# Optimization experiments

Hardware: AMD Instinct MI355X
Metric: run time of the kernel (lower is better)

Reference implementation:

```python
import jax, jax.numpy as jnp
import numpy as np

B2, NC, DIM, H, W = 512, 16, 256, 16, 16


def setup_inputs() -> dict:
    key = jax.random.key(0)
    kf, kr, kc = jax.random.split(key, 3)
    features = jax.random.normal(kf, (B2, DIM, H, W), dtype=jnp.float32)
    # ranking rows are random permutations of class ids 0..NC-1
    perm_keys = jax.random.split(kr, B2)
    ranking = jax.vmap(lambda k: jax.random.permutation(k, NC))(perm_keys).astype(jnp.int32)
    # positive-threshold choice in [1, NC-1] so both arange steps are finite
    choice = jax.random.randint(kc, (B2,), 1, NC, dtype=jnp.int32)
    return {"features": features, "ranking": ranking, "choice": choice, "num_class": NC}


def reference(features, ranking, choice, num_class):
    b2 = features.shape[0]
    x = features.reshape(b2, -1)  # [b2, D]
    sq = jnp.sum(x * x, axis=1)
    dist2 = sq[:, None] + sq[None, :] - 2.0 * (x @ x.T)
    dist = jnp.sqrt(jnp.clip(dist2, 1e-12, None))  # [b2, b2]

    labels = ranking[:, 0]  # pseudo-label of each sample
    # pos[i, c] = rank position j of class c within ranking[i] (inverse permutation)
    pos = jnp.argsort(ranking, axis=1)  # [b2, nc]
    # rank_of_label[i, k] = rank of sample k's label within sample i's ranking
    rank_of_label = pos[:, labels]  # [b2, b2]

    # dic_s[j] = 1 - j/c            for j <  c   (torch.arange(1, 0, -1/c))
    #          = -(j - c + 1)/(nc-c) for j >= c   (torch.arange(-1/(nc-c), -1-1/(nc-c), -1/(nc-c)))
    c = choice[:, None].astype(dist.dtype)  # [b2, 1]
    j = rank_of_label.astype(dist.dtype)
    nc = jnp.asarray(num_class, dist.dtype)
    mask = jnp.where(rank_of_label < choice[:, None],
                     1.0 - j / c,
                     -(j - c + 1.0) / (nc - c))  # [b2, b2]
    # (initial eq-mask is fully overwritten because each ranking row is a full permutation)

    return jnp.mean((dist * mask) ** 2)
```

## Files before the change

kernel.cpp:

```cpp
#include <hip/hip_runtime.h>
#include <hip/hip_bf16.h>

typedef float f32x4 __attribute__((ext_vector_type(4)));
typedef __bf16 bf16x8 __attribute__((ext_vector_type(8)));

constexpr int B2     = 512;
constexpr int KDIM   = 65536;
constexpr int BM     = 256;
constexpr int BK     = 32;
constexpr int NK     = KDIM / BK;
constexpr int KSPLIT = 85;
constexpr int NBLK   = 3 * KSPLIT;

__device__ __forceinline__ void gload16(const void* g, void* l) {
    __builtin_amdgcn_global_load_lds(
        (__attribute__((address_space(1))) void*)(g),
        (__attribute__((address_space(3))) void*)(l), 16, 0, 0);
}

__device__ __forceinline__ void stage_panel(const float* __restrict__ src, int k0,
                                            float* ldsPanel, int tid) {
#pragma unroll
    for (int i = 0; i < 4; ++i) {
        int r    = i * 64 + (tid >> 3);
        int slot = (tid & 7) ^ (r & 7);
        const float* g = src + (size_t)r * KDIM + k0 + slot * 4;
        char* l = (char*)ldsPanel + i * 8192 + (tid & ~63) * 16;
        gload16(g, l);
    }
}

__device__ __forceinline__ bf16x8 read_frag(const char* base, int rowByte, int s0b, int s1b) {
    f32x4 lo = *reinterpret_cast<const f32x4*>(base + rowByte + s0b);
    f32x4 hi = *reinterpret_cast<const f32x4*>(base + rowByte + s1b);
    bf16x8 r;
    r[0] = (__bf16)lo[0]; r[1] = (__bf16)lo[1]; r[2] = (__bf16)lo[2]; r[3] = (__bf16)lo[3];
    r[4] = (__bf16)hi[0]; r[5] = (__bf16)hi[1]; r[6] = (__bf16)hi[2]; r[7] = (__bf16)hi[3];
    return r;
}

__global__ __launch_bounds__(512, 2) void gemm_partial(const float* __restrict__ X,
                                                       __bf16* __restrict__ partials) {
    __shared__ __align__(16) float ldsT[2][2][BM * BK];

    int d = blockIdx.x;
    int xcd = d & 7, slotb = d >> 3;
    int L = (xcd < 7 ? xcd * 32 : 224) + slotb;
    int split = L / 3;
    int tile  = L - split * 3;

    int ti = (tile == 2) ? 1 : 0;
    int tj = (tile == 0) ? 0 : 1;
    bool diag = (ti == tj);
    const float* Abase = X + (size_t)ti * 256 * KDIM;
    const float* Bbase = X + (size_t)tj * 256 * KDIM;

    int tid  = threadIdx.x;
    int lane = tid & 63;
    int wave = tid >> 6;
    int wr = wave >> 2, wc = wave & 3;

    int s0 = split * NK / KSPLIT;
    int s1 = (split + 1) * NK / KSPLIT;

    f32x4 acc[8][4] = {};

    int q  = lane >> 4;
    int rx = lane & 7;
    int s0b = ((2 * q)     ^ rx) * 16;
    int s1b = ((2 * q + 1) ^ rx) * 16;

    stage_panel(Abase, s0 * BK, &ldsT[0][0][0], tid);
    if (!diag) stage_panel(Bbase, s0 * BK, &ldsT[0][1][0], tid);
    __syncthreads();

    int cur = 0;
    for (int s = s0; s < s1; ++s) {
        if (s + 1 < s1) {
            stage_panel(Abase, (s + 1) * BK, &ldsT[cur ^ 1][0][0], tid);
            if (!diag) stage_panel(Bbase, (s + 1) * BK, &ldsT[cur ^ 1][1][0], tid);
        }

        const char* bA = (const char*)&ldsT[cur][0][0];
        const char* bB = diag ? bA : (const char*)&ldsT[cur][1][0];

        bf16x8 bfr[4];
#pragma unroll
        for (int ni = 0; ni < 4; ++ni) {
            int rowB = wc * 64 + ni * 16 + (lane & 15);
            bfr[ni] = read_frag(bB, rowB * 128, s0b, s1b);
        }
#pragma unroll
        for (int mi = 0; mi < 8; ++mi) {
            int rowA = wr * 128 + mi * 16 + (lane & 15);
            bf16x8 a = read_frag(bA, rowA * 128, s0b, s1b);
#pragma unroll
            for (int ni = 0; ni < 4; ++ni)
                acc[mi][ni] = __builtin_amdgcn_mfma_f32_16x16x32_bf16(
                    a, bfr[ni], acc[mi][ni], 0, 0, 0);
        }

        __syncthreads();
        cur ^= 1;
    }

    __bf16* out = partials + (size_t)(tile * KSPLIT + split) * (BM * BM);
    int col = lane & 15, rquad = (lane >> 4) * 4;
#pragma unroll
    for (int mi = 0; mi < 8; ++mi)
#pragma unroll
        for (int ni = 0; ni < 4; ++ni) {
            int j = wc * 64 + ni * 16 + col;
#pragma unroll
            for (int v = 0; v < 4; ++v) {
                int i = wr * 128 + mi * 16 + rquad + v;
                out[i * BM + j] = (__bf16)acc[mi][ni][v];
            }
        }
}

__global__ __launch_bounds__(256) void reduce_partials(const __bf16* __restrict__ partials,
                                                       float* __restrict__ C) {
    int idx  = blockIdx.x * 256 + threadIdx.x;
    int tile = idx / 16384;
    int e4   = idx & 16383;
    const __bf16* p = partials + (size_t)tile * KSPLIT * 65536 + e4 * 4;
    float sx = 0.f, sy = 0.f, sz = 0.f, sw = 0.f;
    for (int s = 0; s < KSPLIT; ++s) {
        ushort4 v = *reinterpret_cast<const ushort4*>(p + (size_t)s * 65536);
        union { unsigned u; float f; } a, b, c2, d2;
        a.u  = (unsigned)v.x << 16;  b.u  = (unsigned)v.y << 16;
        c2.u = (unsigned)v.z << 16;  d2.u = (unsigned)v.w << 16;
        sx += a.f; sy += b.f; sz += c2.f; sw += d2.f;
    }
    int e = e4 * 4;
    int i = e >> 8, j = e & 255;
    int gi = (tile == 2) ? 256 + i : i;
    int gj = (tile == 0) ? j : 256 + j;
    float4 sum = make_float4(sx, sy, sz, sw);
    *reinterpret_cast<float4*>(C + gi * 512 + gj) = sum;
    if (tile == 1) {
        C[(gj + 0) * 512 + gi] = sum.x;
        C[(gj + 1) * 512 + gi] = sum.y;
        C[(gj + 2) * 512 + gi] = sum.z;
        C[(gj + 3) * 512 + gi] = sum.w;
    }
}

__global__ __launch_bounds__(256) void loss_kernel(const float* __restrict__ C,
                                                   const int* __restrict__ ranking,
                                                   const int* __restrict__ choice,
                                                   const int* __restrict__ ncp,
                                                   float* __restrict__ out) {
    __shared__ int pos[16];
    __shared__ float wsum[4];
    int i   = blockIdx.x;
    int tid = threadIdx.x;
    if (tid < 16) pos[ranking[i * 16 + tid]] = tid;
    __syncthreads();

    float nc  = (float)(*ncp);
    int   ci  = choice[i];
    float c   = (float)ci;
    float sqi = C[i * 513];
    float sum = 0.f;

    for (int j = tid; j < B2; j += 256) {
        int   lbl = ranking[j * 16];
        int   r   = pos[lbl];
        float sqj = C[j * 513];
        float d2  = sqi + sqj - 2.f * C[i * 512 + j];
        d2 = fmaxf(d2, 1e-12f);
        float jf = (float)r;
        float m  = (r < ci) ? (1.f - jf / c) : (-(jf - c + 1.f) / (nc - c));
        sum += d2 * m * m;
    }

    for (int off = 32; off > 0; off >>= 1) sum += __shfl_down(sum, off);
    int lane = tid & 63, wave = tid >> 6;
    if (lane == 0) wsum[wave] = sum;
    __syncthreads();
    if (tid == 0) {
        float t = wsum[0] + wsum[1] + wsum[2] + wsum[3];
        atomicAdd(out, t * (1.f / ((float)B2 * (float)B2)));
    }
}

extern "C" void kernel_launch(void* const* d_in, const int* in_sizes, int n_in,
                              void* d_out, int out_size, void* d_ws, size_t ws_size,
                              hipStream_t stream) {
    const float* X       = (const float*)d_in[0];
    const int*   ranking = (const int*)d_in[1];
    const int*   choice  = (const int*)d_in[2];
    const int*   ncp     = (const int*)d_in[3];
    float*       ws      = (float*)d_ws;

    float*  C        = ws;
    __bf16* partials = (__bf16*)(ws + 262144);

    hipMemsetAsync(d_out, 0, sizeof(float), stream);

    gemm_partial<<<dim3(NBLK), dim3(512), 0, stream>>>(X, partials);
    reduce_partials<<<dim3(3 * 16384 / 256), dim3(256), 0, stream>>>(partials, C);
    loss_kernel<<<dim3(B2), dim3(256), 0, stream>>>(C, ranking, choice, ncp, (float*)d_out);
}
```

Measured before the change: 68.00 us.

## Retile Gram GEMM into 128x128 upper-triangle tiles with register-staged bf16 LDS

The 512x512 Gram product now uses ten 128x128 upper-triangular tiles, each split 76 ways along K, replacing three 256x256 tiles with 85 splits. Each block has 256 threads and is bounded to three blocks per CU. Panels are loaded from global memory into registers, converted to bf16 once, and written to a swizzled bf16 LDS buffer, replacing the fp32 direct-to-LDS loads that converted on every fragment read. This halves LDS footprint and adds a register prefetch two steps ahead. The trade-off is more re-reads of X across tiles, plus more partial buffers for the reduce kernel, which now handles the new tile mapping.

```diff
diff --git a/kernel.cpp b/kernel.cpp
--- a/kernel.cpp
+++ b/kernel.cpp
@@ -6,140 +6,144 @@
 
 constexpr int B2     = 512;
 constexpr int KDIM   = 65536;
-constexpr int BM     = 256;
+constexpr int TM     = 128;
 constexpr int BK     = 32;
 constexpr int NK     = KDIM / BK;
-constexpr int KSPLIT = 85;
-constexpr int NBLK   = 3 * KSPLIT;
-
-__device__ __forceinline__ void gload16(const void* g, void* l) {
-    __builtin_amdgcn_global_load_lds(
-        (__attribute__((address_space(1))) void*)(g),
-        (__attribute__((address_space(3))) void*)(l), 16, 0, 0);
-}
-
-__device__ __forceinline__ void stage_panel(const float* __restrict__ src, int k0,
-                                            float* ldsPanel, int tid) {
-#pragma unroll
-    for (int i = 0; i < 4; ++i) {
-        int r    = i * 64 + (tid >> 3);
-        int slot = (tid & 7) ^ (r & 7);
-        const float* g = src + (size_t)r * KDIM + k0 + slot * 4;
-        char* l = (char*)ldsPanel + i * 8192 + (tid & ~63) * 16;
-        gload16(g, l);
-    }
-}
-
-__device__ __forceinline__ bf16x8 read_frag(const char* base, int rowByte, int s0b, int s1b) {
-    f32x4 lo = *reinterpret_cast<const f32x4*>(base + rowByte + s0b);
-    f32x4 hi = *reinterpret_cast<const f32x4*>(base + rowByte + s1b);
-    bf16x8 r;
-    r[0] = (__bf16)lo[0]; r[1] = (__bf16)lo[1]; r[2] = (__bf16)lo[2]; r[3] = (__bf16)lo[3];
-    r[4] = (__bf16)hi[0]; r[5] = (__bf16)hi[1]; r[6] = (__bf16)hi[2]; r[7] = (__bf16)hi[3];
-    return r;
-}
-
-__global__ __launch_bounds__(512, 2) void gemm_partial(const float* __restrict__ X,
+constexpr int NTILE  = 10;
+constexpr int KSPLIT = 76;
+constexpr int NBLK   = NTILE * KSPLIT;
+
+__device__ __forceinline__ void issue_panel(float4* p, const float* __restrict__ src,
+                                            int k0, int tid) {
+    const float* g = src + (size_t)(tid >> 1) * KDIM + k0 + (tid & 1) * 16;
+#pragma unroll
+    for (int it = 0; it < 4; ++it)
+        p[it] = *reinterpret_cast<const float4*>(g + it * 4);
+}
+
+__device__ __forceinline__ void write_panel(__bf16* panel, const float4* p, int tid) {
+    int r = tid >> 1, h = tid & 1;
+    bf16x8 v0, v1;
+    v0[0] = (__bf16)p[0].x; v0[1] = (__bf16)p[0].y; v0[2] = (__bf16)p[0].z; v0[3] = (__bf16)p[0].w;
+    v0[4] = (__bf16)p[1].x; v0[5] = (__bf16)p[1].y; v0[6] = (__bf16)p[1].z; v0[7] = (__bf16)p[1].w;
+    v1[0] = (__bf16)p[2].x; v1[1] = (__bf16)p[2].y; v1[2] = (__bf16)p[2].z; v1[3] = (__bf16)p[2].w;
+    v1[4] = (__bf16)p[3].x; v1[5] = (__bf16)p[3].y; v1[6] = (__bf16)p[3].z; v1[7] = (__bf16)p[3].w;
+    char* base = reinterpret_cast<char*>(panel) + r * 64;
+    *reinterpret_cast<bf16x8*>(base + (((2 * h)     ^ (r & 3)) * 16)) = v0;
+    *reinterpret_cast<bf16x8*>(base + (((2 * h + 1) ^ (r & 3)) * 16)) = v1;
+}
+
+__device__ __forceinline__ void lds_barrier() {
+    asm volatile("s_waitcnt lgkmcnt(0)" ::: "memory");
+    __builtin_amdgcn_s_barrier();
+}
+
+__global__ __launch_bounds__(256, 3) void gemm_partial(const float* __restrict__ X,
                                                        __bf16* __restrict__ partials) {
-    __shared__ __align__(16) float ldsT[2][2][BM * BK];
+    __shared__ __align__(16) __bf16 lds[2][2][TM * BK];
 
     int d = blockIdx.x;
-    int xcd = d & 7, slotb = d >> 3;
-    int L = (xcd < 7 ? xcd * 32 : 224) + slotb;
-    int split = L / 3;
-    int tile  = L - split * 3;
-
-    int ti = (tile == 2) ? 1 : 0;
-    int tj = (tile == 0) ? 0 : 1;
-    bool diag = (ti == tj);
-    const float* Abase = X + (size_t)ti * 256 * KDIM;
-    const float* Bbase = X + (size_t)tj * 256 * KDIM;
+    int L = (d & 7) * 95 + (d >> 3);
+    int split = L / NTILE;
+    int t     = L - split * NTILE;
+    int i = (t >= 9) ? 3 : (t >= 7) ? 2 : (t >= 4) ? 1 : 0;
+    int j = t - ((i == 0) ? 0 : (i == 1) ? 3 : (i == 2) ? 5 : 6);
+    bool diag = (i == j);
+    const float* Abase = X + (size_t)i * TM * KDIM;
+    const float* Bbase = X + (size_t)j * TM * KDIM;
 
     int tid  = threadIdx.x;
     int lane = tid & 63;
     int wave = tid >> 6;
-    int wr = wave >> 2, wc = wave & 3;
+    int wr = wave >> 1, wc = wave & 1;
 
     int s0 = split * NK / KSPLIT;
     int s1 = (split + 1) * NK / KSPLIT;
 
-    f32x4 acc[8][4] = {};
-
-    int q  = lane >> 4;
-    int rx = lane & 7;
-    int s0b = ((2 * q)     ^ rx) * 16;
-    int s1b = ((2 * q + 1) ^ rx) * 16;
-
-    stage_panel(Abase, s0 * BK, &ldsT[0][0][0], tid);
-    if (!diag) stage_panel(Bbase, s0 * BK, &ldsT[0][1][0], tid);
-    __syncthreads();
-
-    int cur = 0;
+    f32x4 acc[4][4] = {};
+    float4 pa[4], pb[4];
+
+    int pslot  = ((lane >> 4) ^ (lane & 3)) * 16;
+    int rbyteA = (wr * 64 + (lane & 15)) * 64 + pslot;
+    int rbyteB = (wc * 64 + (lane & 15)) * 64 + pslot;
+
+    issue_panel(pa, Abase, s0 * BK, tid);
+    if (!diag) issue_panel(pb, Bbase, s0 * BK, tid);
+    write_panel(&lds[0][0][0], pa, tid);
+    if (!diag) write_panel(&lds[0][1][0], pb, tid);
+    if (s0 + 1 < s1) {
+        issue_panel(pa, Abase, (s0 + 1) * BK, tid);
+        if (!diag) issue_panel(pb, Bbase, (s0 + 1) * BK, tid);
+    }
+    lds_barrier();
+
     for (int s = s0; s < s1; ++s) {
-        if (s + 1 < s1) {
-            stage_panel(Abase, (s + 1) * BK, &ldsT[cur ^ 1][0][0], tid);
-            if (!diag) stage_panel(Bbase, (s + 1) * BK, &ldsT[cur ^ 1][1][0], tid);
-        }
-
-        const char* bA = (const char*)&ldsT[cur][0][0];
-        const char* bB = diag ? bA : (const char*)&ldsT[cur][1][0];
+        int cur = (s - s0) & 1;
+        const char* bA = (const char*)&lds[cur][0][0];
+        const char* bB = diag ? bA : (const char*)&lds[cur][1][0];
 
         bf16x8 bfr[4];
 #pragma unroll
-        for (int ni = 0; ni < 4; ++ni) {
-            int rowB = wc * 64 + ni * 16 + (lane & 15);
-            bfr[ni] = read_frag(bB, rowB * 128, s0b, s1b);
-        }
-#pragma unroll
-        for (int mi = 0; mi < 8; ++mi) {
-            int rowA = wr * 128 + mi * 16 + (lane & 15);
-            bf16x8 a = read_frag(bA, rowA * 128, s0b, s1b);
+        for (int ni = 0; ni < 4; ++ni)
+            bfr[ni] = *reinterpret_cast<const bf16x8*>(bB + rbyteB + ni * 1024);
+#pragma unroll
+        for (int mi = 0; mi < 4; ++mi) {
+            bf16x8 a = *reinterpret_cast<const bf16x8*>(bA + rbyteA + mi * 1024);
 #pragma unroll
             for (int ni = 0; ni < 4; ++ni)
                 acc[mi][ni] = __builtin_amdgcn_mfma_f32_16x16x32_bf16(
                     a, bfr[ni], acc[mi][ni], 0, 0, 0);
         }
 
-        __syncthreads();
-        cur ^= 1;
-    }
-
-    __bf16* out = partials + (size_t)(tile * KSPLIT + split) * (BM * BM);
-    int col = lane & 15, rquad = (lane >> 4) * 4;
-#pragma unroll
-    for (int mi = 0; mi < 8; ++mi)
-#pragma unroll
-        for (int ni = 0; ni < 4; ++ni) {
-            int j = wc * 64 + ni * 16 + col;
-#pragma unroll
-            for (int v = 0; v < 4; ++v) {
-                int i = wr * 128 + mi * 16 + rquad + v;
-                out[i * BM + j] = (__bf16)acc[mi][ni][v];
+        if (s + 1 < s1) {
+            write_panel(&lds[cur ^ 1][0][0], pa, tid);
+            if (!diag) write_panel(&lds[cur ^ 1][1][0], pb, tid);
+            if (s + 2 < s1) {
+                issue_panel(pa, Abase, (s + 2) * BK, tid);
+                if (!diag) issue_panel(pb, Bbase, (s + 2) * BK, tid);
             }
         }
+        lds_barrier();
+    }
+
+    __bf16* out = partials + (size_t)(t * KSPLIT + split) * (TM * TM);
+    int col = lane & 15, rquad = (lane >> 4) * 4;
+#pragma unroll
+    for (int mi = 0; mi < 4; ++mi)
+#pragma unroll
+        for (int ni = 0; ni < 4; ++ni) {
+            int cj = wc * 64 + ni * 16 + col;
+#pragma unroll
+            for (int v = 0; v < 4; ++v) {
+                int ri = wr * 64 + mi * 16 + rquad + v;
+                out[ri * TM + cj] = (__bf16)acc[mi][ni][v];
+            }
+        }
 }
 
 __global__ __launch_bounds__(256) void reduce_partials(const __bf16* __restrict__ partials,
                                                        float* __restrict__ C) {
-    int idx  = blockIdx.x * 256 + threadIdx.x;
-    int tile = idx / 16384;
-    int e4   = idx & 16383;
-    const __bf16* p = partials + (size_t)tile * KSPLIT * 65536 + e4 * 4;
+    int idx = blockIdx.x * 256 + threadIdx.x;
+    int t   = idx / 4096;
+    int e4  = idx & 4095;
+    int r   = e4 >> 5;
+    int c4  = e4 & 31;
+    const __bf16* src = partials + (size_t)t * KSPLIT * (TM * TM) + r * TM + c4 * 4;
     float sx = 0.f, sy = 0.f, sz = 0.f, sw = 0.f;
     for (int s = 0; s < KSPLIT; ++s) {
-        ushort4 v = *reinterpret_cast<const ushort4*>(p + (size_t)s * 65536);
+        ushort4 v = *reinterpret_cast<const ushort4*>(src + (size_t)s * (TM * TM));
         union { unsigned u; float f; } a, b, c2, d2;
         a.u  = (unsigned)v.x << 16;  b.u  = (unsigned)v.y << 16;
         c2.u = (unsigned)v.z << 16;  d2.u = (unsigned)v.w << 16;
         sx += a.f; sy += b.f; sz += c2.f; sw += d2.f;
     }
-    int e = e4 * 4;
-    int i = e >> 8, j = e & 255;
-    int gi = (tile == 2) ? 256 + i : i;
-    int gj = (tile == 0) ? j : 256 + j;
+    int i = (t >= 9) ? 3 : (t >= 7) ? 2 : (t >= 4) ? 1 : 0;
+    int j = t - ((i == 0) ? 0 : (i == 1) ? 3 : (i == 2) ? 5 : 6);
+    int gi = i * TM + r;
+    int gj = j * TM + c4 * 4;
     float4 sum = make_float4(sx, sy, sz, sw);
     *reinterpret_cast<float4*>(C + gi * 512 + gj) = sum;
-    if (tile == 1) {
+    if (i != j) {
         C[(gj + 0) * 512 + gi] = sum.x;
         C[(gj + 1) * 512 + gi] = sum.y;
         C[(gj + 2) * 512 + gi] = sum.z;
@@ -181,8 +185,8 @@
     if (lane == 0) wsum[wave] = sum;
     __syncthreads();
     if (tid == 0) {
-        float t = wsum[0] + wsum[1] + wsum[2] + wsum[3];
-        atomicAdd(out, t * (1.f / ((float)B2 * (float)B2)));
+        float tsum = wsum[0] + wsum[1] + wsum[2] + wsum[3];
+        atomicAdd(out, tsum * (1.f / ((float)B2 * (float)B2)));
     }
 }
 
@@ -200,7 +204,7 @@
 
     hipMemsetAsync(d_out, 0, sizeof(float), stream);
 
-    gemm_partial<<<dim3(NBLK), dim3(512), 0, stream>>>(X, partials);
-    reduce_partials<<<dim3(3 * 16384 / 256), dim3(256), 0, stream>>>(partials, C);
+    gemm_partial<<<dim3(NBLK), dim3(256), 0, stream>>>(X, partials);
+    reduce_partials<<<dim3(NTILE * 4096 / 256), dim3(256), 0, stream>>>(partials, C);
     loss_kernel<<<dim3(B2), dim3(256), 0, stream>>>(C, ranking, choice, ncp, (float*)d_out);
 }
```

Measured after the change: 76.06 us. 1.12x slower.

## Interleave next-tile global loads with MFMA phases in the GEMM main loop

Applied to the files above, without the earlier changes.

The GEMM inner loop is restructured into four phases. Each phase issues one quarter of the next K-panel's global-to-LDS loads, then runs two rows of MFMAs under raised wave priority (s_setprio). The single __syncthreads at the end of each iteration is replaced by an explicit vmcnt wait plus barrier at the top and extra s_barriers between phases. The aim is to spread memory traffic across the compute and keep the matrix units busy. The extra barriers and manual waitcnts add synchronization cost and need correct ordering to avoid LDS races.

```diff
diff --git a/kernel.cpp b/kernel.cpp
--- a/kernel.cpp
+++ b/kernel.cpp
@@ -18,16 +18,12 @@
         (__attribute__((address_space(3))) void*)(l), 16, 0, 0);
 }
 
-__device__ __forceinline__ void stage_panel(const float* __restrict__ src, int k0,
-                                            float* ldsPanel, int tid) {
-#pragma unroll
-    for (int i = 0; i < 4; ++i) {
-        int r    = i * 64 + (tid >> 3);
-        int slot = (tid & 7) ^ (r & 7);
-        const float* g = src + (size_t)r * KDIM + k0 + slot * 4;
-        char* l = (char*)ldsPanel + i * 8192 + (tid & ~63) * 16;
-        gload16(g, l);
-    }
+__device__ __forceinline__ void stage_q(const float* __restrict__ src, int k0,
+                                        float* ldsPanel, int tid, int it) {
+    int r    = it * 64 + (tid >> 3);
+    int slot = (tid & 7) ^ (r & 7);
+    gload16(src + (size_t)r * KDIM + k0 + slot * 4,
+            (char*)ldsPanel + it * 8192 + (tid & ~63) * 16);
 }
 
 __device__ __forceinline__ bf16x8 read_frag(const char* base, int rowByte, int s0b, int s1b) {
@@ -69,39 +65,95 @@
     int rx = lane & 7;
     int s0b = ((2 * q)     ^ rx) * 16;
     int s1b = ((2 * q + 1) ^ rx) * 16;
-
-    stage_panel(Abase, s0 * BK, &ldsT[0][0][0], tid);
-    if (!diag) stage_panel(Bbase, s0 * BK, &ldsT[0][1][0], tid);
-    __syncthreads();
-
-    int cur = 0;
+    int rA0 = (wr * 128 + (lane & 15)) * 128;
+    int rB0 = (wc * 64  + (lane & 15)) * 128;
+
+#pragma unroll
+    for (int it = 0; it < 4; ++it) {
+        stage_q(Abase, s0 * BK, &ldsT[0][0][0], tid, it);
+        if (!diag) stage_q(Bbase, s0 * BK, &ldsT[0][1][0], tid, it);
+    }
+
     for (int s = s0; s < s1; ++s) {
-        if (s + 1 < s1) {
-            stage_panel(Abase, (s + 1) * BK, &ldsT[cur ^ 1][0][0], tid);
-            if (!diag) stage_panel(Bbase, (s + 1) * BK, &ldsT[cur ^ 1][1][0], tid);
-        }
-
+        int cur = (s - s0) & 1;
         const char* bA = (const char*)&ldsT[cur][0][0];
         const char* bB = diag ? bA : (const char*)&ldsT[cur][1][0];
+        float* nA = &ldsT[cur ^ 1][0][0];
+        float* nB = &ldsT[cur ^ 1][1][0];
+        bool pre = (s + 1 < s1);
+        int nk0 = (s + 1) * BK;
+
+        asm volatile("s_waitcnt vmcnt(0)" ::: "memory");
+        __builtin_amdgcn_s_barrier();
 
         bf16x8 bfr[4];
 #pragma unroll
-        for (int ni = 0; ni < 4; ++ni) {
-            int rowB = wc * 64 + ni * 16 + (lane & 15);
-            bfr[ni] = read_frag(bB, rowB * 128, s0b, s1b);
-        }
-#pragma unroll
-        for (int mi = 0; mi < 8; ++mi) {
-            int rowA = wr * 128 + mi * 16 + (lane & 15);
-            bf16x8 a = read_frag(bA, rowA * 128, s0b, s1b);
-#pragma unroll
-            for (int ni = 0; ni < 4; ++ni)
-                acc[mi][ni] = __builtin_amdgcn_mfma_f32_16x16x32_bf16(
-                    a, bfr[ni], acc[mi][ni], 0, 0, 0);
-        }
-
-        __syncthreads();
-        cur ^= 1;
+        for (int ni = 0; ni < 4; ++ni)
+            bfr[ni] = read_frag(bB, rB0 + ni * 2048, s0b, s1b);
+        bf16x8 a0 = read_frag(bA, rA0 + 0 * 2048, s0b, s1b);
+        bf16x8 a1 = read_frag(bA, rA0 + 1 * 2048, s0b, s1b);
+        if (pre) {
+            stage_q(Abase, nk0, nA, tid, 0);
+            if (!diag) stage_q(Bbase, nk0, nB, tid, 0);
+            stage_q(Abase, nk0, nA, tid, 1);
+            if (!diag) stage_q(Bbase, nk0, nB, tid, 1);
+        }
+        asm volatile("s_waitcnt lgkmcnt(0)" ::: "memory");
+        __builtin_amdgcn_s_setprio(1);
+#pragma unroll
+        for (int ni = 0; ni < 4; ++ni)
+            acc[0][ni] = __builtin_amdgcn_mfma_f32_16x16x32_bf16(a0, bfr[ni], acc[0][ni], 0, 0, 0);
+#pragma unroll
+        for (int ni = 0; ni < 4; ++ni)
+            acc[1][ni] = __builtin_amdgcn_mfma_f32_16x16x32_bf16(a1, bfr[ni], acc[1][ni], 0, 0, 0);
+        __builtin_amdgcn_s_setprio(0);
+        a0 = read_frag(bA, rA0 + 2 * 2048, s0b, s1b);
+        a1 = read_frag(bA, rA0 + 3 * 2048, s0b, s1b);
+        __builtin_amdgcn_s_barrier();
+
+        if (pre) {
+            stage_q(Abase, nk0, nA, tid, 2);
+            if (!diag) stage_q(Bbase, nk0, nB, tid, 2);
+        }
+        asm volatile("s_waitcnt lgkmcnt(0)" ::: "memory");
+        __builtin_amdgcn_s_setprio(1);
+#pragma unroll
+        for (int ni = 0; ni < 4; ++ni)
+            acc[2][ni] = __builtin_amdgcn_mfma_f32_16x16x32_bf16(a0, bfr[ni], acc[2][ni], 0, 0, 0);
+#pragma unroll
+        for (int ni = 0; ni < 4; ++ni)
+            acc[3][ni] = __builtin_amdgcn_mfma_f32_16x16x32_bf16(a1, bfr[ni], acc[3][ni], 0, 0, 0);
+        __builtin_amdgcn_s_setprio(0);
+        a0 = read_frag(bA, rA0 + 4 * 2048, s0b, s1b);
+        a1 = read_frag(bA, rA0 + 5 * 2048, s0b, s1b);
+        __builtin_amdgcn_s_barrier();
+
+        if (pre) {
+            stage_q(Abase, nk0, nA, tid, 3);
+            if (!diag) stage_q(Bbase, nk0, nB, tid, 3);
+        }
+        asm volatile("s_waitcnt lgkmcnt(0)" ::: "memory");
+        __builtin_amdgcn_s_setprio(1);
+#pragma unroll
+        for (int ni = 0; ni < 4; ++ni)
+            acc[4][ni] = __builtin_amdgcn_mfma_f32_16x16x32_bf16(a0, bfr[ni], acc[4][ni], 0, 0, 0);
+#pragma unroll
+        for (int ni = 0; ni < 4; ++ni)
+            acc[5][ni] = __builtin_amdgcn_mfma_f32_16x16x32_bf16(a1, bfr[ni], acc[5][ni], 0, 0, 0);
+        __builtin_amdgcn_s_setprio(0);
+        a0 = read_frag(bA, rA0 + 6 * 2048, s0b, s1b);
+        a1 = read_frag(bA, rA0 + 7 * 2048, s0b, s1b);
+        __builtin_amdgcn_s_barrier();
+
+        asm volatile("s_waitcnt lgkmcnt(0)" ::: "memory");
+        __builtin_amdgcn_s_setprio(1);
+#pragma unroll
+        for (int ni = 0; ni < 4; ++ni)
+            acc[6][ni] = __builtin_amdgcn_mfma_f32_16x16x32_bf16(a0, bfr[ni], acc[6][ni], 0, 0, 0);
+#pragma unroll
+        for (int ni = 0; ni < 4; ++ni)
+            acc[7][ni] = __builtin_amdgcn_mfma_f32_16x16x32_bf16(a1, bfr[ni], acc[7][ni], 0, 0, 0);
+        __builtin_amdgcn_s_setprio(0);
     }
 
     __bf16* out = partials + (size_t)(tile * KSPLIT + split) * (BM * BM);
```

After: 69.14 us. About the same (+1.7%).

## Replace Gram GEMM with algebraic low-rank decomposition over label classes

Applied to the files above, without the earlier changes.

Rewrites the loss algebraically: because the mask depends only on row i's rank of sample k's label (16 classes), the weighted sum of squared distances splits into per-row norm terms and a 16-class cross term. A prep kernel builds the squared-mask table and per-row weights, and a single column pass streams X once, accumulating per-class weighted and label-grouped sums. This removes the 512x512 bf16 MFMA GEMM, the partials buffer and its reduction, and runs in fp32 instead of bf16. It drops the clamp at 1e-12 on squared distances, which only matters for near-identical rows, and relies on float atomics, so summation order is nondeterministic.

```diff
diff --git a/kernel.cpp b/kernel.cpp
--- a/kernel.cpp
+++ b/kernel.cpp
@@ -1,189 +1,137 @@
 #include <hip/hip_runtime.h>
-#include <hip/hip_bf16.h>
 
-typedef float f32x4 __attribute__((ext_vector_type(4)));
-typedef __bf16 bf16x8 __attribute__((ext_vector_type(8)));
 
-constexpr int B2     = 512;
-constexpr int KDIM   = 65536;
-constexpr int BM     = 256;
-constexpr int BK     = 32;
-constexpr int NK     = KDIM / BK;
-constexpr int KSPLIT = 85;
-constexpr int NBLK   = 3 * KSPLIT;
+constexpr int NROW = 512;
+constexpr int KDIM = 65536;
 
-__device__ __forceinline__ void gload16(const void* g, void* l) {
-    __builtin_amdgcn_global_load_lds(
-        (__attribute__((address_space(1))) void*)(g),
-        (__attribute__((address_space(3))) void*)(l), 16, 0, 0);
+__global__ __launch_bounds__(512) void prep_kernel(const int* __restrict__ ranking,
+                                                   const int* __restrict__ choice,
+                                                   const int* __restrict__ ncp,
+                                                   float* __restrict__ g2,
+                                                   float2* __restrict__ utab) {
+    __shared__ float Hs[16];
+    __shared__ int   cnt[16];
+    int i = threadIdx.x;
+    if (i < 16) { Hs[i] = 0.f; cnt[i] = 0; }
+    __syncthreads();
+
+    int rk[16];
+#pragma unroll
+    for (int q = 0; q < 16; ++q) rk[q] = ranking[i * 16 + q];
+    int pos[16];
+#pragma unroll
+    for (int q = 0; q < 16; ++q) pos[rk[q]] = q;
+
+    int   lbl = rk[0];
+    float c   = (float)choice[i];
+    float nc  = (float)(*ncp);
+    atomicAdd(&cnt[lbl], 1);
+
+    float grow[16];
+#pragma unroll
+    for (int q = 0; q < 16; ++q) {
+        float r = (float)pos[q];
+        float m = (r < c) ? (1.f - r / c) : (-(r - c + 1.f) / (nc - c));
+        grow[q] = m * m;
+        g2[i * 16 + q] = grow[q];
+        atomicAdd(&Hs[q], grow[q]);
+    }
+    __syncthreads();
+
+    float u = 0.f;
+#pragma unroll
+    for (int q = 0; q < 16; ++q) u += (float)cnt[q] * grow[q];
+    u += Hs[lbl];
+    utab[i] = make_float2(u, __int_as_float(lbl));
 }
 
-__device__ __forceinline__ void stage_panel(const float* __restrict__ src, int k0,
-                                            float* ldsPanel, int tid) {
+__global__ __launch_bounds__(256, 2) void colpass(const float* __restrict__ X,
+                                                  const float* __restrict__ g2,
+                                                  const float2* __restrict__ utab,
+                                                  float* __restrict__ acc) {
+    __shared__ float xch[128][33];
+    __shared__ float red[8];
+
+    int t = threadIdx.x;
+    int k = blockIdx.x * 128 + (t & 127);
+    int row0 = __builtin_amdgcn_readfirstlane((t >> 7) * 256);
+    const float* xp = X + (size_t)row0 * KDIM + k;
+
+    float w[16] = {};
+    float s[16] = {};
+    float t1 = 0.f;
+
+#pragma unroll 4
+    for (int r = 0; r < 256; ++r) {
+        float x = xp[(size_t)r * KDIM];
+        int row = row0 + r;
+        float2 ul = utab[row];
+        int lbl = __float_as_int(ul.y);
+        const float4* g4 = reinterpret_cast<const float4*>(g2 + row * 16);
+        float4 ga = g4[0], gb = g4[1], gc = g4[2], gd = g4[3];
+
+        w[0]  = fmaf(ga.x, x, w[0]);  w[1]  = fmaf(ga.y, x, w[1]);
+        w[2]  = fmaf(ga.z, x, w[2]);  w[3]  = fmaf(ga.w, x, w[3]);
+        w[4]  = fmaf(gb.x, x, w[4]);  w[5]  = fmaf(gb.y, x, w[5]);
+        w[6]  = fmaf(gb.z, x, w[6]);  w[7]  = fmaf(gb.w, x, w[7]);
+        w[8]  = fmaf(gc.x, x, w[8]);  w[9]  = fmaf(gc.y, x, w[9]);
+        w[10] = fmaf(gc.z, x, w[10]); w[11] = fmaf(gc.w, x, w[11]);
+        w[12] = fmaf(gd.x, x, w[12]); w[13] = fmaf(gd.y, x, w[13]);
+        w[14] = fmaf(gd.z, x, w[14]); w[15] = fmaf(gd.w, x, w[15]);
+
+        switch (lbl) {
+            case 0:  s[0]  += x; break;
+            case 1:  s[1]  += x; break;
+            case 2:  s[2]  += x; break;
+            case 3:  s[3]  += x; break;
+            case 4:  s[4]  += x; break;
+            case 5:  s[5]  += x; break;
+            case 6:  s[6]  += x; break;
+            case 7:  s[7]  += x; break;
+            case 8:  s[8]  += x; break;
+            case 9:  s[9]  += x; break;
+            case 10: s[10] += x; break;
+            case 11: s[11] += x; break;
+            case 12: s[12] += x; break;
+            case 13: s[13] += x; break;
+            case 14: s[14] += x; break;
+            default: s[15] += x; break;
+        }
+        t1 = fmaf(ul.x, x * x, t1);
+    }
+
+    if (t < 128) {
 #pragma unroll
-    for (int i = 0; i < 4; ++i) {
-        int r    = i * 64 + (tid >> 3);
-        int slot = (tid & 7) ^ (r & 7);
-        const float* g = src + (size_t)r * KDIM + k0 + slot * 4;
-        char* l = (char*)ldsPanel + i * 8192 + (tid & ~63) * 16;
-        gload16(g, l);
+        for (int c = 0; c < 16; ++c) { xch[t][c] = w[c]; xch[t][16 + c] = s[c]; }
+    }
+    __syncthreads();
+    float cp = 0.f;
+    if (t >= 128) {
+        int p = t - 128;
+#pragma unroll
+        for (int c = 0; c < 16; ++c) {
+            float wt = w[c] + xch[p][c];
+            float st = s[c] + xch[p][16 + c];
+            cp = fmaf(wt, st, cp);
+        }
+    }
+
+#pragma unroll
+    for (int off = 32; off > 0; off >>= 1) {
+        cp += __shfl_down(cp, off);
+        t1 += __shfl_down(t1, off);
+    }
+    int wv = t >> 6;
+    if ((t & 63) == 0) { red[wv] = cp; red[4 + wv] = t1; }
+    __syncthreads();
+    if (t == 0) {
+        atomicAdd(&acc[1], red[0] + red[1] + red[2] + red[3]);
+        atomicAdd(&acc[0], red[4] + red[5] + red[6] + red[7]);
     }
 }
 
-__device__ __forceinline__ bf16x8 read_frag(const char* base, int rowByte, int s0b, int s1b) {
-    f32x4 lo = *reinterpret_cast<const f32x4*>(base + rowByte + s0b);
-    f32x4 hi = *reinterpret_cast<const f32x4*>(base + rowByte + s1b);
-    bf16x8 r;
-    r[0] = (__bf16)lo[0]; r[1] = (__bf16)lo[1]; r[2] = (__bf16)lo[2]; r[3] = (__bf16)lo[3];
-    r[4] = (__bf16)hi[0]; r[5] = (__bf16)hi[1]; r[6] = (__bf16)hi[2]; r[7] = (__bf16)hi[3];
-    return r;
-}
-
-__global__ __launch_bounds__(512, 2) void gemm_partial(const float* __restrict__ X,
-                                                       __bf16* __restrict__ partials) {
-    __shared__ __align__(16) float ldsT[2][2][BM * BK];
-
-    int d = blockIdx.x;
-    int xcd = d & 7, slotb = d >> 3;
-    int L = (xcd < 7 ? xcd * 32 : 224) + slotb;
-    int split = L / 3;
-    int tile  = L - split * 3;
-
-    int ti = (tile == 2) ? 1 : 0;
-    int tj = (tile == 0) ? 0 : 1;
-    bool diag = (ti == tj);
-    const float* Abase = X + (size_t)ti * 256 * KDIM;
-    const float* Bbase = X + (size_t)tj * 256 * KDIM;
-
-    int tid  = threadIdx.x;
-    int lane = tid & 63;
-    int wave = tid >> 6;
-    int wr = wave >> 2, wc = wave & 3;
-
-    int s0 = split * NK / KSPLIT;
-    int s1 = (split + 1) * NK / KSPLIT;
-
-    f32x4 acc[8][4] = {};
-
-    int q  = lane >> 4;
-    int rx = lane & 7;
-    int s0b = ((2 * q)     ^ rx) * 16;
-    int s1b = ((2 * q + 1) ^ rx) * 16;
-
-    stage_panel(Abase, s0 * BK, &ldsT[0][0][0], tid);
-    if (!diag) stage_panel(Bbase, s0 * BK, &ldsT[0][1][0], tid);
-    __syncthreads();
-
-    int cur = 0;
-    for (int s = s0; s < s1; ++s) {
-        if (s + 1 < s1) {
-            stage_panel(Abase, (s + 1) * BK, &ldsT[cur ^ 1][0][0], tid);
-            if (!diag) stage_panel(Bbase, (s + 1) * BK, &ldsT[cur ^ 1][1][0], tid);
-        }
-
-        const char* bA = (const char*)&ldsT[cur][0][0];
-        const char* bB = diag ? bA : (const char*)&ldsT[cur][1][0];
-
-        bf16x8 bfr[4];
-#pragma unroll
-        for (int ni = 0; ni < 4; ++ni) {
-            int rowB = wc * 64 + ni * 16 + (lane & 15);
-            bfr[ni] = read_frag(bB, rowB * 128, s0b, s1b);
-        }
-#pragma unroll
-        for (int mi = 0; mi < 8; ++mi) {
-            int rowA = wr * 128 + mi * 16 + (lane & 15);
-            bf16x8 a = read_frag(bA, rowA * 128, s0b, s1b);
-#pragma unroll
-            for (int ni = 0; ni < 4; ++ni)
-                acc[mi][ni] = __builtin_amdgcn_mfma_f32_16x16x32_bf16(
-                    a, bfr[ni], acc[mi][ni], 0, 0, 0);
-        }
-
-        __syncthreads();
-        cur ^= 1;
-    }
-
-    __bf16* out = partials + (size_t)(tile * KSPLIT + split) * (BM * BM);
-    int col = lane & 15, rquad = (lane >> 4) * 4;
-#pragma unroll
-    for (int mi = 0; mi < 8; ++mi)
-#pragma unroll
-        for (int ni = 0; ni < 4; ++ni) {
-            int j = wc * 64 + ni * 16 + col;
-#pragma unroll
-            for (int v = 0; v < 4; ++v) {
-                int i = wr * 128 + mi * 16 + rquad + v;
-                out[i * BM + j] = (__bf16)acc[mi][ni][v];
-            }
-        }
-}
-
-__global__ __launch_bounds__(256) void reduce_partials(const __bf16* __restrict__ partials,
-                                                       float* __restrict__ C) {
-    int idx  = blockIdx.x * 256 + threadIdx.x;
-    int tile = idx / 16384;
-    int e4   = idx & 16383;
-    const __bf16* p = partials + (size_t)tile * KSPLIT * 65536 + e4 * 4;
-    float sx = 0.f, sy = 0.f, sz = 0.f, sw = 0.f;
-    for (int s = 0; s < KSPLIT; ++s) {
-        ushort4 v = *reinterpret_cast<const ushort4*>(p + (size_t)s * 65536);
-        union { unsigned u; float f; } a, b, c2, d2;
-        a.u  = (unsigned)v.x << 16;  b.u  = (unsigned)v.y << 16;
-        c2.u = (unsigned)v.z << 16;  d2.u = (unsigned)v.w << 16;
-        sx += a.f; sy += b.f; sz += c2.f; sw += d2.f;
-    }
-    int e = e4 * 4;
-    int i = e >> 8, j = e & 255;
-    int gi = (tile == 2) ? 256 + i : i;
-    int gj = (tile == 0) ? j : 256 + j;
-    float4 sum = make_float4(sx, sy, sz, sw);
-    *reinterpret_cast<float4*>(C + gi * 512 + gj) = sum;
-    if (tile == 1) {
-        C[(gj + 0) * 512 + gi] = sum.x;
-        C[(gj + 1) * 512 + gi] = sum.y;
-        C[(gj + 2) * 512 + gi] = sum.z;
-        C[(gj + 3) * 512 + gi] = sum.w;
-    }
-}
-
-__global__ __launch_bounds__(256) void loss_kernel(const float* __restrict__ C,
-                                                   const int* __restrict__ ranking,
-                                                   const int* __restrict__ choice,
-                                                   const int* __restrict__ ncp,
-                                                   float* __restrict__ out) {
-    __shared__ int pos[16];
-    __shared__ float wsum[4];
-    int i   = blockIdx.x;
-    int tid = threadIdx.x;
-    if (tid < 16) pos[ranking[i * 16 + tid]] = tid;
-    __syncthreads();
-
-    float nc  = (float)(*ncp);
-    int   ci  = choice[i];
-    float c   = (float)ci;
-    float sqi = C[i * 513];
-    float sum = 0.f;
-
-    for (int j = tid; j < B2; j += 256) {
-        int   lbl = ranking[j * 16];
-        int   r   = pos[lbl];
-        float sqj = C[j * 513];
-        float d2  = sqi + sqj - 2.f * C[i * 512 + j];
-        d2 = fmaxf(d2, 1e-12f);
-        float jf = (float)r;
-        float m  = (r < ci) ? (1.f - jf / c) : (-(jf - c + 1.f) / (nc - c));
-        sum += d2 * m * m;
-    }
-
-    for (int off = 32; off > 0; off >>= 1) sum += __shfl_down(sum, off);
-    int lane = tid & 63, wave = tid >> 6;
-    if (lane == 0) wsum[wave] = sum;
-    __syncthreads();
-    if (tid == 0) {
-        float t = wsum[0] + wsum[1] + wsum[2] + wsum[3];
-        atomicAdd(out, t * (1.f / ((float)B2 * (float)B2)));
-    }
+__global__ void finalize(const float* __restrict__ acc, float* __restrict__ out) {
+    out[0] = (acc[0] - 2.f * acc[1]) * (1.f / ((float)NROW * (float)NROW));
 }
 
 extern "C" void kernel_launch(void* const* d_in, const int* in_sizes, int n_in,
@@ -195,12 +143,12 @@
     const int*   ncp     = (const int*)d_in[3];
     float*       ws      = (float*)d_ws;
 
-    float*  C        = ws;
-    __bf16* partials = (__bf16*)(ws + 262144);
+    float*  acc  = ws;
+    float*  g2   = ws + 4;
+    float2* utab = (float2*)(ws + 4 + NROW * 16);
 
-    hipMemsetAsync(d_out, 0, sizeof(float), stream);
-
-    gemm_partial<<<dim3(NBLK), dim3(512), 0, stream>>>(X, partials);
-    reduce_partials<<<dim3(3 * 16384 / 256), dim3(256), 0, stream>>>(partials, C);
-    loss_kernel<<<dim3(B2), dim3(256), 0, stream>>>(C, ranking, choice, ncp, (float*)d_out);
+    hipMemsetAsync(acc, 0, 2 * sizeof(float), stream);
+    prep_kernel<<<dim3(1), dim3(512), 0, stream>>>(ranking, choice, ncp, g2, utab);
+    colpass<<<dim3(512), dim3(256), 0, stream>>>(X, g2, utab, acc);
+    finalize<<<dim3(1), dim3(1), 0, stream>>>(acc, (float*)d_out);
 }
```

Result: slower. 124.2 us (+82.7%).
